# Optimization experiments

Hardware: AMD Instinct MI355X
Metric: run time of the kernel (lower is better)

The kernel has to match this reference:

```python
import jax, jax.numpy as jnp
import numpy as np

N_NODES = 100000
N_EDGES = 1600000
K = 48

def setup_inputs() -> dict:
    key = jax.random.key(0)
    ks = jax.random.split(key, 6)
    x = jax.random.normal(ks[0], (N_NODES, K), dtype=jnp.float32)
    pos_edge_index = jax.random.randint(ks[1], (2, N_EDGES), 0, N_NODES, dtype=jnp.int64)
    neg_edge_index = jax.random.randint(ks[2], (2, N_EDGES), 0, N_NODES, dtype=jnp.int64)
    # nn.Linear-style init (uniform +-1/sqrt(fan_in))
    lim1 = 1.0 / np.sqrt(3 * K)
    W1 = jax.random.uniform(ks[3], (3 * K, 16), minval=-lim1, maxval=lim1, dtype=jnp.float32)
    b1 = jnp.zeros((16,), dtype=jnp.float32)
    lim2 = 1.0 / np.sqrt(16)
    W2 = jax.random.uniform(ks[4], (16, K), minval=-lim2, maxval=lim2, dtype=jnp.float32)
    b2 = jnp.zeros((K,), dtype=jnp.float32)
    return {"x": x, "pos_edge_index": pos_edge_index, "neg_edge_index": neg_edge_index,
            "W1": W1, "b1": b1, "W2": W2, "b2": b2}

def _scatter_add_mp(x, edge_index):
    # PyG MessagePassing(aggr='add'), message = x_j:
    # gather source-node features and scatter-add into target nodes.
    src, dst = edge_index[0], edge_index[1]
    msgs = x[src]  # [E, k]
    return jax.ops.segment_sum(msgs, dst, num_segments=x.shape[0])  # [N, k]

def reference(x, pos_edge_index, neg_edge_index, W1, b1, W2, b2):
    x_pos = _scatter_add_mp(x, pos_edge_index)
    x_neg = _scatter_add_mp(x, neg_edge_index)
    out_cat = jnp.concatenate([x, x_pos, x_neg], axis=1)  # [N, 3k]
    h = jnp.tanh(out_cat @ W1 + b1)                        # [N, 16]
    C = h @ W2 + b2                                        # [N, k]
    return jax.nn.softmax(C, axis=1)
```

## Files before the change

kernel.cpp:

```cpp
#include <hip/hip_runtime.h>
#include <hip/hip_fp16.h>
#include <math.h>

#define NN 100000
#define NE 1600000
#define KF 48
#define NEDGE_ALL (2 * NE)

#define BKT_NODES 128
#define NBKT_PER  782
#define NBKT      1564
#define PACK_EPB  16384
#define STG_HALF  8192
#define NPB       196
#define OT2       1566
#define OTT       200
#define CAP2      2432
#define KSTG      10

typedef _Float16 half2v __attribute__((ext_vector_type(2)));
typedef _Float16 half4v __attribute__((ext_vector_type(4)));
typedef _Float16 half8v __attribute__((ext_vector_type(8)));

#if defined(__has_builtin)
#if __has_builtin(__builtin_amdgcn_fdot2)
#define HAVE_FDOT2 1
#endif
#endif

__device__ __forceinline__ void acc_pair(float& ax, float& ay, half2v v)
{
#ifdef HAVE_FDOT2
    ax = __builtin_amdgcn_fdot2(v, (half2v){(_Float16)1.f, (_Float16)0.f}, ax, false);
    ay = __builtin_amdgcn_fdot2(v, (half2v){(_Float16)0.f, (_Float16)1.f}, ay, false);
#else
    ax += (float)v.x;
    ay += (float)v.y;
#endif
}

__global__ __launch_bounds__(512) void pack_kernel(
    const float* __restrict__ x,
    const int* __restrict__ ei_pos,
    const int* __restrict__ ei_neg,
    const float* __restrict__ W1,
    const float* __restrict__ b1,
    unsigned short* __restrict__ offT,
    unsigned* __restrict__ plist,
    float* __restrict__ za,
    __half* __restrict__ zbh,
    __half* __restrict__ zch)
{
    __shared__ int cnt[NBKT];
    __shared__ int ps[391];
    __shared__ unsigned stage[STG_HALF];
    __shared__ float sW1[144 * 16];
    __shared__ float sb1[16];

    const int t = threadIdx.x;
    for (int i = t; i < 144 * 16; i += 512) sW1[i] = W1[i];
    if (t < 16) sb1[t] = b1[t];
    for (int i = t; i < NBKT; i += 512) cnt[i] = 0;
    __syncthreads();

    {
        const int n = blockIdx.x * 512 + t;
        if (n < NN + 2) {
            float aA[16], aB[16], aC[16];
#pragma unroll
            for (int j = 0; j < 16; ++j) { aA[j] = sb1[j]; aB[j] = 0.f; aC[j] = 0.f; }
            if (n < NN) {
                const float4* __restrict__ x4 = (const float4*)(x + (long)n * KF);
                for (int i4 = 0; i4 < 12; ++i4) {
                    float4 v = x4[i4];
                    float vv[4] = {v.x, v.y, v.z, v.w};
#pragma unroll
                    for (int c = 0; c < 4; ++c) {
                        const int f = i4 * 4 + c;
                        const float* wA = &sW1[f * 16];
                        const float* wB = &sW1[(48 + f) * 16];
                        const float* wC = &sW1[(96 + f) * 16];
                        const float s = vv[c];
#pragma unroll
                        for (int j = 0; j < 16; ++j) {
                            aA[j] += s * wA[j];
                            aB[j] += s * wB[j];
                            aC[j] += s * wC[j];
                        }
                    }
                }
                float4* za4 = (float4*)(za + (long)n * 16);
#pragma unroll
                for (int j4 = 0; j4 < 4; ++j4)
                    za4[j4] = make_float4(aA[4*j4], aA[4*j4+1], aA[4*j4+2], aA[4*j4+3]);
            }
            half8v hb0, hb1, hc0, hc1;
#pragma unroll
            for (int j = 0; j < 8; ++j) {
                hb0[j] = (_Float16)aB[j];     hb1[j] = (_Float16)aB[8 + j];
                hc0[j] = (_Float16)aC[j];     hc1[j] = (_Float16)aC[8 + j];
            }
            half8v* zb8 = (half8v*)zbh;
            half8v* zc8 = (half8v*)zch;
            zb8[(long)n * 2 + 0] = hb0;  zb8[(long)n * 2 + 1] = hb1;
            zc8[(long)n * 2 + 0] = hc0;  zc8[(long)n * 2 + 1] = hc1;
        }
    }

    unsigned pk[32];
    int bk[32];
    const int blockBase = blockIdx.x * PACK_EPB;
#pragma unroll
    for (int j = 0; j < 32; ++j) {
        int e = blockBase + j * 512 + t;
        bk[j] = -1;
        if (e < NEDGE_ALL) {
            int list = e >= NE;
            int ee = list ? e - NE : e;
            const int* ei = list ? ei_neg : ei_pos;
            int src = ei[ee];
            int dst = ei[NE + ee];
            int b = list * NBKT_PER + (dst >> 7);
            bk[j] = b;
            pk[j] = ((unsigned)(dst & 127) << 17) | (unsigned)src;
            atomicAdd(&cnt[b], 1);
        }
    }
    __syncthreads();

    int s0 = 0, s1 = 0, s2 = 0, s3 = 0;
    if (t < 391) {
        s0 = cnt[4 * t]; s1 = cnt[4 * t + 1]; s2 = cnt[4 * t + 2]; s3 = cnt[4 * t + 3];
        ps[t] = s0 + s1 + s2 + s3;
    }
    __syncthreads();
    for (int d = 1; d < 391; d <<= 1) {
        int v = (t < 391 && t >= d) ? ps[t - d] : 0;
        __syncthreads();
        if (t < 391) ps[t] += v;
        __syncthreads();
    }
    unsigned short* myrow = offT + (long)blockIdx.x * OT2;
    if (t < 391) {
        int base = t ? ps[t - 1] : 0;
        int o0 = base, o1 = o0 + s0, o2 = o1 + s1, o3 = o2 + s2;
        myrow[4 * t]     = (unsigned short)o0;
        myrow[4 * t + 1] = (unsigned short)o1;
        myrow[4 * t + 2] = (unsigned short)o2;
        myrow[4 * t + 3] = (unsigned short)o3;
        cnt[4 * t] = o0; cnt[4 * t + 1] = o1; cnt[4 * t + 2] = o2; cnt[4 * t + 3] = o3;
    }
    if (t == 390) myrow[NBKT] = (unsigned short)ps[390];
    __syncthreads();

#pragma unroll
    for (int j = 0; j < 32; ++j) {
        if (bk[j] >= 0)
            bk[j] = atomicAdd(&cnt[bk[j]], 1);
    }

#pragma unroll
    for (int j = 0; j < 32; ++j) {
        if (bk[j] >= 0 && bk[j] < STG_HALF)
            stage[bk[j]] = pk[j];
    }
    __syncthreads();
    {
        const uint4* __restrict__ st4 = (const uint4*)stage;
        uint4* __restrict__ out4 = (uint4*)(plist + (long)blockIdx.x * PACK_EPB);
#pragma unroll
        for (int j = 0; j < 4; ++j)
            out4[j * 512 + t] = st4[j * 512 + t];
    }
    __syncthreads();

#pragma unroll
    for (int j = 0; j < 32; ++j) {
        if (bk[j] >= STG_HALF)
            stage[bk[j] - STG_HALF] = pk[j];
    }
    __syncthreads();
    {
        const uint4* __restrict__ st4 = (const uint4*)stage;
        uint4* __restrict__ out4 = (uint4*)(plist + (long)blockIdx.x * PACK_EPB + STG_HALF);
#pragma unroll
        for (int j = 0; j < 4; ++j)
            out4[j * 512 + t] = st4[j * 512 + t];
    }
}

__global__ __launch_bounds__(256) void transposeT_kernel(
    const unsigned short* __restrict__ offT,
    unsigned short* __restrict__ offTT)
{
    __shared__ unsigned short tile[64][NPB + 6];
    const int t = threadIdx.x;
    const int b0 = blockIdx.x * 64;

    for (int idx = t; idx < 64 * NPB; idx += 256) {
        int r = idx >> 6;
        int c = idx & 63;
        int b = b0 + c;
        tile[c][r] = (b <= NBKT) ? offT[(long)r * OT2 + b] : (unsigned short)0;
    }
    __syncthreads();
    for (int idx = t; idx < 64 * NPB; idx += 256) {
        int c = idx / NPB;
        int r = idx - c * NPB;
        int b = b0 + c;
        if (b <= NBKT) offTT[(long)b * OTT + r] = tile[c][r];
    }
}

__global__ __launch_bounds__(256) void gather_kernel(
    const __half* __restrict__ zbh,
    const __half* __restrict__ zch,
    const unsigned* __restrict__ plist,
    const unsigned short* __restrict__ offTT,
    float* __restrict__ hpos,
    float* __restrict__ hneg)
{
    __shared__ unsigned srt[CAP2];
    __shared__ int rb[NPB + 2];
    __shared__ int sc[NPB];
    __shared__ unsigned short rsL[NPB];
    __shared__ int nh[BKT_NODES];
    __shared__ int starts[BKT_NODES];
    __shared__ int ends[BKT_NODES];
    __shared__ int cur2[BKT_NODES];

    const int bid = blockIdx.x;
    const int xcd = bid & 7;
    const int slot = bid >> 3;
    const int list = xcd >> 2;
    const int nb = slot * 4 + (xcd & 3);
    if (nb >= NBKT_PER) return;
    const int b = list * NBKT_PER + nb;

    const int t = threadIdx.x;

    if (t < NPB) {
        int s = offTT[(long)b * OTT + t];
        int e = offTT[(long)(b + 1) * OTT + t];
        rsL[t] = (unsigned short)s;
        sc[t] = e - s;
    }
    if (t < BKT_NODES) nh[t] = 0;
    __syncthreads();

    for (int d = 1; d < NPB; d <<= 1) {
        int v = (t < NPB && t >= d) ? sc[t - d] : 0;
        __syncthreads();
        if (t < NPB) sc[t] += v;
        __syncthreads();
    }
    if (t < NPB) rb[t + 1] = sc[t];
    if (t == 0) rb[0] = 0;
    __syncthreads();
    int cb = rb[NPB];
    if (cb > CAP2) cb = CAP2;

    unsigned held[KSTG];
#pragma unroll
    for (int k = 0; k < KSTG; ++k) {
        int i = t + k * 256;
        held[k] = 0;
        if (i < cb) {
            int lo = 0, hi = NPB - 1;
#pragma unroll
            for (int it = 0; it < 8; ++it) {
                int mid = (lo + hi + 1) >> 1;
                bool ge = (rb[mid] <= i);
                lo = ge ? mid : lo;
                hi = ge ? hi : mid - 1;
            }
            unsigned p = plist[(long)lo * PACK_EPB + rsL[lo] + (i - rb[lo])];
            held[k] = p;
            atomicAdd(&nh[p >> 17], 1);
        }
    }
    __syncthreads();

    for (int d = 1; d < BKT_NODES; d <<= 1) {
        int v = 0;
        if (t < BKT_NODES && t >= d) v = nh[t - d];
        __syncthreads();
        if (t < BKT_NODES) nh[t] += v;
        __syncthreads();
    }
    if (t < BKT_NODES) {
        int e_ = min(nh[t], CAP2);
        int s_ = t ? min(nh[t - 1], CAP2) : 0;
        starts[t] = s_;
        ends[t] = e_;
        cur2[t] = s_;
    }
    __syncthreads();

#pragma unroll
    for (int k = 0; k < KSTG; ++k) {
        int i = t + k * 256;
        if (i < cb) {
            unsigned p = held[k];
            int slot2 = atomicAdd(&cur2[p >> 17], 1);
            if (slot2 < CAP2) srt[slot2] = p;
        }
    }
    __syncthreads();

    const int wave = t >> 6, lane = t & 63;
    const int g = lane >> 2;
    const int sub = lane & 3;
    float* o = list ? hneg : hpos;
    const half4v* __restrict__ z4 = (const half4v*)(list ? zch : zbh);

    for (int n = wave; n < BKT_NODES; n += 4) {
        int gn = nb * BKT_NODES + n;
        if (gn >= NN) continue;
        int s = starts[n], e = ends[n];
        float a0 = 0.f, a1 = 0.f, a2 = 0.f, a3 = 0.f;
        for (int j = s; j < e; j += 16) {
            int i0 = j + g;
            int q = (i0 < e) ? (int)(srt[i0 < CAP2 ? i0 : 0] & 0x1FFFFu) : NN;
            half4v v = z4[q * 4 + sub];
            acc_pair(a0, a1, (half2v){v.x, v.y});
            acc_pair(a2, a3, (half2v){v.z, v.w});
        }
        a0 += __shfl_xor(a0, 4); a0 += __shfl_xor(a0, 8); a0 += __shfl_xor(a0, 16); a0 += __shfl_xor(a0, 32);
        a1 += __shfl_xor(a1, 4); a1 += __shfl_xor(a1, 8); a1 += __shfl_xor(a1, 16); a1 += __shfl_xor(a1, 32);
        a2 += __shfl_xor(a2, 4); a2 += __shfl_xor(a2, 8); a2 += __shfl_xor(a2, 16); a2 += __shfl_xor(a2, 32);
        a3 += __shfl_xor(a3, 4); a3 += __shfl_xor(a3, 8); a3 += __shfl_xor(a3, 16); a3 += __shfl_xor(a3, 32);
        if (g == 0) {
            float4* o4 = (float4*)o;
            o4[(long)gn * 4 + sub] = make_float4(a0, a1, a2, a3);
        }
    }
}

__global__ __launch_bounds__(256) void mlp2_kernel(
    const float* __restrict__ za,
    const float* __restrict__ hpos,
    const float* __restrict__ hneg,
    const float* __restrict__ W2,
    const float* __restrict__ b2,
    float* __restrict__ out)
{
    __shared__ float sW2[16 * 48];
    __shared__ float sb2[48];
    for (int i = threadIdx.x; i < 16 * 48; i += 256) sW2[i] = W2[i];
    if (threadIdx.x < 48) sb2[threadIdx.x] = b2[threadIdx.x];
    __syncthreads();

    const int n = blockIdx.x * 256 + threadIdx.x;
    if (n >= NN) return;

    const float4* A = (const float4*)(za   + (long)n * 16);
    const float4* P = (const float4*)(hpos + (long)n * 16);
    const float4* Q = (const float4*)(hneg + (long)n * 16);
    float h[16];
#pragma unroll
    for (int j4 = 0; j4 < 4; ++j4) {
        float4 a = A[j4], p = P[j4], q = Q[j4];
        h[4 * j4 + 0] = tanhf(a.x + p.x + q.x);
        h[4 * j4 + 1] = tanhf(a.y + p.y + q.y);
        h[4 * j4 + 2] = tanhf(a.z + p.z + q.z);
        h[4 * j4 + 3] = tanhf(a.w + p.w + q.w);
    }

    float C[KF];
#pragma unroll
    for (int k = 0; k < KF; ++k) C[k] = sb2[k];
    for (int j = 0; j < 16; ++j) {
        const float hv = h[j];
        const float* w = &sW2[j * KF];
#pragma unroll
        for (int k = 0; k < KF; ++k) C[k] += hv * w[k];
    }

    float m = C[0];
#pragma unroll
    for (int k = 1; k < KF; ++k) m = fmaxf(m, C[k]);
    float ssum = 0.f;
#pragma unroll
    for (int k = 0; k < KF; ++k) { C[k] = expf(C[k] - m); ssum += C[k]; }
    const float inv = 1.0f / ssum;

    float4* po = (float4*)(out + (long)n * KF);
#pragma unroll
    for (int k4 = 0; k4 < 12; ++k4)
        po[k4] = make_float4(C[4*k4] * inv, C[4*k4+1] * inv, C[4*k4+2] * inv, C[4*k4+3] * inv);
}

__global__ __launch_bounds__(256) void scatter2_kernel(
    const float* __restrict__ x,
    const int* __restrict__ ei_pos,
    const int* __restrict__ ei_neg,
    float* acc_pos,
    float* acc_neg)
{
    const int list = blockIdx.y;
    const int* ei = list ? ei_neg : ei_pos;
    float* acc = list ? acc_neg : acc_pos;

    long t = (long)blockIdx.x * blockDim.x + threadIdx.x;
    const long total = (long)NE * 12;
    if (t >= total) return;

    int e = (int)(t / 12);
    int r = (int)(t - (long)e * 12);
    int k4 = r * 4;

    int src = ei[e];
    int dst = ei[NE + e];

    const float4 v = *(const float4*)(x + (long)src * KF + k4);
    float* p = acc + (long)dst * KF + k4;

    unsafeAtomicAdd(p + 0, v.x);
    unsafeAtomicAdd(p + 1, v.y);
    unsafeAtomicAdd(p + 2, v.z);
    unsafeAtomicAdd(p + 3, v.w);
}

__global__ __launch_bounds__(256) void mlp_softmax_kernel(
    const float* __restrict__ x,
    const float* xpos,
    const float* __restrict__ xneg,
    const float* __restrict__ W1,
    const float* __restrict__ b1,
    const float* __restrict__ W2,
    const float* __restrict__ b2,
    float* out)
{
    __shared__ float sW1[144 * 16];
    __shared__ float sW2[16 * 48];
    __shared__ float sb1[16];
    __shared__ float sb2[48];

    for (int i = threadIdx.x; i < 144 * 16; i += blockDim.x) sW1[i] = W1[i];
    for (int i = threadIdx.x; i < 16 * 48;  i += blockDim.x) sW2[i] = W2[i];
    if (threadIdx.x < 16) sb1[threadIdx.x] = b1[threadIdx.x];
    if (threadIdx.x < 48) sb2[threadIdx.x] = b2[threadIdx.x];
    __syncthreads();

    const int n = blockIdx.x * blockDim.x + threadIdx.x;
    if (n >= NN) return;

    float h[16];
#pragma unroll
    for (int j = 0; j < 16; ++j) h[j] = sb1[j];

    const float* srcs[3];
    srcs[0] = x    + (long)n * KF;
    srcs[1] = xpos + (long)n * KF;
    srcs[2] = xneg + (long)n * KF;

    for (int s = 0; s < 3; ++s) {
        const float* px = srcs[s];
        for (int i = 0; i < KF; ++i) {
            const float v = px[i];
            const float* w = &sW1[(s * KF + i) * 16];
#pragma unroll
            for (int j = 0; j < 16; ++j) h[j] += v * w[j];
        }
    }
#pragma unroll
    for (int j = 0; j < 16; ++j) h[j] = tanhf(h[j]);

    float C[KF];
#pragma unroll
    for (int k = 0; k < KF; ++k) C[k] = sb2[k];
    for (int j = 0; j < 16; ++j) {
        const float hv = h[j];
        const float* w = &sW2[j * KF];
#pragma unroll
        for (int k = 0; k < KF; ++k) C[k] += hv * w[k];
    }

    float m = C[0];
#pragma unroll
    for (int k = 1; k < KF; ++k) m = fmaxf(m, C[k]);
    float ssum = 0.f;
#pragma unroll
    for (int k = 0; k < KF; ++k) { C[k] = expf(C[k] - m); ssum += C[k]; }
    const float inv = 1.0f / ssum;

    float* po = out + (long)n * KF;
#pragma unroll
    for (int k = 0; k < KF; ++k) po[k] = C[k] * inv;
}

extern "C" void kernel_launch(void* const* d_in, const int* in_sizes, int n_in,
                              void* d_out, int out_size, void* d_ws, size_t ws_size,
                              hipStream_t stream)
{
    const float* x      = (const float*)d_in[0];
    const int*   ei_pos = (const int*)  d_in[1];
    const int*   ei_neg = (const int*)  d_in[2];
    const float* W1     = (const float*)d_in[3];
    const float* b1     = (const float*)d_in[4];
    const float* W2     = (const float*)d_in[5];
    const float* b2     = (const float*)d_in[6];

    float* out = (float*)d_out;

    const size_t h_bytes     = (size_t)NN * 16 * sizeof(float);
    const size_t za_bytes    = (size_t)NN * 16 * sizeof(float);
    const size_t zh_bytes    = (size_t)(NN + 2) * 16 * sizeof(__half);
    const size_t plist_bytes = (size_t)NPB * PACK_EPB * sizeof(unsigned);
    const size_t offT_bytes  = (size_t)NPB * OT2 * sizeof(unsigned short);
    const size_t offTT_bytes = (size_t)(NBKT + 2) * OTT * sizeof(unsigned short);

    size_t off = 0;
    char* ws = (char*)d_ws;
    float*          hpos  = (float*)(ws + off);          off += h_bytes;
    float*          hneg  = (float*)(ws + off);          off += h_bytes;
    float*          za    = (float*)(ws + off);          off += za_bytes;
    __half*         zbh   = (__half*)(ws + off);         off += zh_bytes;
    __half*         zch   = (__half*)(ws + off);         off += zh_bytes;
    unsigned*       plist = (unsigned*)(ws + off);       off += plist_bytes;
    unsigned short* offT  = (unsigned short*)(ws + off); off += offT_bytes;
    unsigned short* offTT = (unsigned short*)(ws + off); off += offTT_bytes;
    const size_t needed = off;

    if (ws_size >= needed) {
        pack_kernel<<<NPB, 512, 0, stream>>>(x, ei_pos, ei_neg, W1, b1, offT, plist, za, zbh, zch);
        transposeT_kernel<<<(NBKT + 1 + 63) / 64, 256, 0, stream>>>(offT, offTT);
        gather_kernel<<<196 * 8, 256, 0, stream>>>(zbh, zch, plist, offTT, hpos, hneg);
        mlp2_kernel<<<(NN + 255) / 256, 256, 0, stream>>>(za, hpos, hneg, W2, b2, out);
    } else {
        float* xpos = (float*)d_out;
        float* xneg = (float*)d_ws;
        const size_t acc_bytes = (size_t)NN * KF * sizeof(float);
        hipMemsetAsync(xpos, 0, acc_bytes, stream);
        hipMemsetAsync(xneg, 0, acc_bytes, stream);
        const long total = (long)NE * 12;
        dim3 grid((unsigned)((total + 255) / 256), 2, 1);
        scatter2_kernel<<<grid, 256, 0, stream>>>(x, ei_pos, ei_neg, xpos, xneg);
        mlp_softmax_kernel<<<(NN + 255) / 256, 256, 0, stream>>>(x, xpos, xneg, W1, b1, W2, b2, out);
    }
}
```

Before: 223.4 us.

## Replace per-bucket counting sort in gather with LDS float atomic accumulation

The gather kernel no longer sorts bucket edges by destination node through a histogram, a scan and a scatter into LDS before segmented reduction. Each thread now handles one edge, loads the 16 half source features and atomically adds them into a transposed LDS accumulator (16 x 132 floats, padded stride) indexed by destination node. The accumulator is then written out as float4 rows. This drops several syncthreads and scans, and also lifts the CAP2 truncation, but adds 16 LDS float atomics per edge, which may contend on hot nodes, and makes summation order nondeterministic.

```diff
diff --git a/kernel.cpp b/kernel.cpp
--- a/kernel.cpp
+++ b/kernel.cpp
@@ -15,29 +15,11 @@
 #define NPB       196
 #define OT2       1566
 #define OTT       200
-#define CAP2      2432
-#define KSTG      10
+#define HSTR      132
 
 typedef _Float16 half2v __attribute__((ext_vector_type(2)));
 typedef _Float16 half4v __attribute__((ext_vector_type(4)));
 typedef _Float16 half8v __attribute__((ext_vector_type(8)));
-
-#if defined(__has_builtin)
-#if __has_builtin(__builtin_amdgcn_fdot2)
-#define HAVE_FDOT2 1
-#endif
-#endif
-
-__device__ __forceinline__ void acc_pair(float& ax, float& ay, half2v v)
-{
-#ifdef HAVE_FDOT2
-    ax = __builtin_amdgcn_fdot2(v, (half2v){(_Float16)1.f, (_Float16)0.f}, ax, false);
-    ay = __builtin_amdgcn_fdot2(v, (half2v){(_Float16)0.f, (_Float16)1.f}, ay, false);
-#else
-    ax += (float)v.x;
-    ay += (float)v.y;
-#endif
-}
 
 __global__ __launch_bounds__(512) void pack_kernel(
     const float* __restrict__ x,
@@ -220,14 +202,10 @@
     float* __restrict__ hpos,
     float* __restrict__ hneg)
 {
-    __shared__ unsigned srt[CAP2];
+    __shared__ float hacc[16 * HSTR];
     __shared__ int rb[NPB + 2];
     __shared__ int sc[NPB];
     __shared__ unsigned short rsL[NPB];
-    __shared__ int nh[BKT_NODES];
-    __shared__ int starts[BKT_NODES];
-    __shared__ int ends[BKT_NODES];
-    __shared__ int cur2[BKT_NODES];
 
     const int bid = blockIdx.x;
     const int xcd = bid & 7;
@@ -245,7 +223,7 @@
         rsL[t] = (unsigned short)s;
         sc[t] = e - s;
     }
-    if (t < BKT_NODES) nh[t] = 0;
+    for (int i = t; i < 16 * HSTR; i += 256) hacc[i] = 0.f;
     __syncthreads();
 
     for (int d = 1; d < NPB; d <<= 1) {
@@ -257,82 +235,46 @@
     if (t < NPB) rb[t + 1] = sc[t];
     if (t == 0) rb[0] = 0;
     __syncthreads();
-    int cb = rb[NPB];
-    if (cb > CAP2) cb = CAP2;
-
-    unsigned held[KSTG];
-#pragma unroll
-    for (int k = 0; k < KSTG; ++k) {
-        int i = t + k * 256;
-        held[k] = 0;
-        if (i < cb) {
-            int lo = 0, hi = NPB - 1;
-#pragma unroll
-            for (int it = 0; it < 8; ++it) {
-                int mid = (lo + hi + 1) >> 1;
-                bool ge = (rb[mid] <= i);
-                lo = ge ? mid : lo;
-                hi = ge ? hi : mid - 1;
-            }
-            unsigned p = plist[(long)lo * PACK_EPB + rsL[lo] + (i - rb[lo])];
-            held[k] = p;
-            atomicAdd(&nh[p >> 17], 1);
+    const int cb = rb[NPB];
+
+    const __half* __restrict__ zt = list ? zch : zbh;
+
+    for (int i = t; i < cb; i += 256) {
+        int lo = 0, hi = NPB - 1;
+#pragma unroll
+        for (int it = 0; it < 8; ++it) {
+            int mid = (lo + hi + 1) >> 1;
+            bool ge = (rb[mid] <= i);
+            lo = ge ? mid : lo;
+            hi = ge ? hi : mid - 1;
         }
-    }
-    __syncthreads();
-
-    for (int d = 1; d < BKT_NODES; d <<= 1) {
-        int v = 0;
-        if (t < BKT_NODES && t >= d) v = nh[t - d];
-        __syncthreads();
-        if (t < BKT_NODES) nh[t] += v;
-        __syncthreads();
-    }
-    if (t < BKT_NODES) {
-        int e_ = min(nh[t], CAP2);
-        int s_ = t ? min(nh[t - 1], CAP2) : 0;
-        starts[t] = s_;
-        ends[t] = e_;
-        cur2[t] = s_;
-    }
-    __syncthreads();
-
-#pragma unroll
-    for (int k = 0; k < KSTG; ++k) {
-        int i = t + k * 256;
-        if (i < cb) {
-            unsigned p = held[k];
-            int slot2 = atomicAdd(&cur2[p >> 17], 1);
-            if (slot2 < CAP2) srt[slot2] = p;
-        }
-    }
-    __syncthreads();
-
-    const int wave = t >> 6, lane = t & 63;
-    const int g = lane >> 2;
-    const int sub = lane & 3;
-    float* o = list ? hneg : hpos;
-    const half4v* __restrict__ z4 = (const half4v*)(list ? zch : zbh);
-
-    for (int n = wave; n < BKT_NODES; n += 4) {
-        int gn = nb * BKT_NODES + n;
-        if (gn >= NN) continue;
-        int s = starts[n], e = ends[n];
-        float a0 = 0.f, a1 = 0.f, a2 = 0.f, a3 = 0.f;
-        for (int j = s; j < e; j += 16) {
-            int i0 = j + g;
-            int q = (i0 < e) ? (int)(srt[i0 < CAP2 ? i0 : 0] & 0x1FFFFu) : NN;
-            half4v v = z4[q * 4 + sub];
-            acc_pair(a0, a1, (half2v){v.x, v.y});
-            acc_pair(a2, a3, (half2v){v.z, v.w});
-        }
-        a0 += __shfl_xor(a0, 4); a0 += __shfl_xor(a0, 8); a0 += __shfl_xor(a0, 16); a0 += __shfl_xor(a0, 32);
-        a1 += __shfl_xor(a1, 4); a1 += __shfl_xor(a1, 8); a1 += __shfl_xor(a1, 16); a1 += __shfl_xor(a1, 32);
-        a2 += __shfl_xor(a2, 4); a2 += __shfl_xor(a2, 8); a2 += __shfl_xor(a2, 16); a2 += __shfl_xor(a2, 32);
-        a3 += __shfl_xor(a3, 4); a3 += __shfl_xor(a3, 8); a3 += __shfl_xor(a3, 16); a3 += __shfl_xor(a3, 32);
-        if (g == 0) {
-            float4* o4 = (float4*)o;
-            o4[(long)gn * 4 + sub] = make_float4(a0, a1, a2, a3);
+        unsigned p = plist[(long)lo * PACK_EPB + rsL[lo] + (i - rb[lo])];
+        int node = (int)(p >> 17);
+        int src  = (int)(p & 0x1FFFFu);
+        const half8v* __restrict__ z8 = (const half8v*)(zt + (long)src * 16);
+        half8v z0 = z8[0];
+        half8v z1 = z8[1];
+#pragma unroll
+        for (int k = 0; k < 8; ++k) atomicAdd(&hacc[k * HSTR + node],       (float)z0[k]);
+#pragma unroll
+        for (int k = 0; k < 8; ++k) atomicAdd(&hacc[(8 + k) * HSTR + node], (float)z1[k]);
+    }
+    __syncthreads();
+
+    {
+        const int node = t >> 1;
+        const int hh = t & 1;
+        const int gn = nb * BKT_NODES + node;
+        if (gn < NN) {
+            const int k0 = hh * 8;
+            float4 v0 = make_float4(hacc[k0 * HSTR + node],       hacc[(k0 + 1) * HSTR + node],
+                                    hacc[(k0 + 2) * HSTR + node], hacc[(k0 + 3) * HSTR + node]);
+            float4 v1 = make_float4(hacc[(k0 + 4) * HSTR + node], hacc[(k0 + 5) * HSTR + node],
+                                    hacc[(k0 + 6) * HSTR + node], hacc[(k0 + 7) * HSTR + node]);
+            float* o = list ? hneg : hpos;
+            float4* o4 = (float4*)(o + (long)gn * 16);
+            o4[hh * 2]     = v0;
+            o4[hh * 2 + 1] = v1;
         }
     }
 }
```

Result: slower. 467.0 us (+109.1%).
